# Kernel optimization log

Measured on AMD Instinct MI355X. Metric: run time of the kernel, lower is better.

The kernel has to match this reference:

```python
import jax, jax.numpy as jnp
import numpy as np
import math

N_EMBD = 2048
N_HEAD = 16
HEAD_DIM = N_EMBD // N_HEAD  # 128
K = 8
P = 2
B = 1
T = 2048
EPS = 1e-6


def _rms_norm(x):
    return x * jax.lax.rsqrt(jnp.mean(x * x, axis=-1, keepdims=True) + EPS)


def _rope(x, cos, sin):
    # x: [B, T, H, D]; cos/sin: [T, D//2]
    d = x.shape[-1] // 2
    x1, x2 = x[..., :d], x[..., d:]
    c = cos[None, :, None, :]
    s = sin[None, :, None, :]
    return jnp.concatenate([x1 * c + x2 * s, -x1 * s + x2 * c], axis=-1)


def setup_inputs() -> dict:
    key = jax.random.key(0)
    ks = jax.random.split(key, 8)
    x = jax.random.normal(ks[0], (B, T, N_EMBD), jnp.float32)
    half = HEAD_DIM // 2
    inv_freq = 1.0 / (10000.0 ** (np.arange(half, dtype=np.float32) / half))
    ang = np.arange(T, dtype=np.float32)[:, None] * inv_freq[None, :]
    cos = jnp.asarray(np.cos(ang), jnp.float32)
    sin = jnp.asarray(np.sin(ang), jnp.float32)
    sc = 1.0 / math.sqrt(N_EMBD)
    Wq = jax.random.normal(ks[1], (N_EMBD, N_EMBD), jnp.float32) * sc
    Wk = jax.random.normal(ks[2], (N_EMBD, N_EMBD), jnp.float32) * sc
    Wv = jax.random.normal(ks[3], (N_EMBD, N_EMBD), jnp.float32) * sc
    Wproj = jax.random.normal(ks[4], (N_EMBD, N_EMBD), jnp.float32) * sc
    scd = 1.0 / math.sqrt(HEAD_DIM)
    Wdq = jax.random.normal(ks[5], (K, HEAD_DIM), jnp.float32) * scd
    Wdk = jax.random.normal(ks[6], (K, HEAD_DIM), jnp.float32) * scd
    return {"x": x, "cos": cos, "sin": sin, "Wq": Wq, "Wk": Wk, "Wv": Wv, "Wproj": Wproj, "Wdq": Wdq, "Wdk": Wdk}


def reference(x, cos, sin, Wq, Wk, Wv, Wproj, Wdq, Wdk):
    Bq, Tq, C = x.shape
    q = (x @ Wq.T).reshape(Bq, Tq, N_HEAD, HEAD_DIM)
    k = (x @ Wk.T).reshape(Bq, Tq, N_HEAD, HEAD_DIM)
    v = (x @ Wv.T).reshape(Bq, Tq, N_HEAD, HEAD_DIM)
    q = _rms_norm(_rope(q, cos, sin))
    k = _rms_norm(_rope(k, cos, sin))
    q = jnp.swapaxes(q, 1, 2)  # [B,H,T,D]
    k = jnp.swapaxes(k, 1, 2)
    v = jnp.swapaxes(v, 1, 2)
    # base-p digits in {0..p-1}; p=2 -> bits
    qd = jnp.floor(jax.nn.sigmoid(jnp.einsum('bhtd,kd->bhtk', q, Wdq)) * (P - 0.01)).astype(jnp.int32)
    kd = jnp.floor(jax.nn.sigmoid(jnp.einsum('bhtd,kd->bhtk', k, Wdk)) * (P - 0.01)).astype(jnp.int32)
    # lcp >= K-1  <=>  first K-1 digits all equal; pack them into one code
    pw = (P ** jnp.arange(K - 1)).astype(jnp.int32)  # [K-1]
    qc = jnp.sum(qd[..., : K - 1] * pw, axis=-1)  # [B,H,T]
    kc = jnp.sum(kd[..., : K - 1] * pw, axis=-1)
    lcp_mask = qc[..., :, None] == kc[..., None, :]  # [B,H,Tq,Tk]
    causal = jnp.tril(jnp.ones((Tq, Tq), dtype=bool))
    mask = lcp_mask & causal
    scores = jnp.einsum('bhqd,bhkd->bhqk', q, k) * (1.0 / math.sqrt(HEAD_DIM))
    s = jnp.where(mask, scores, -1e30)
    w = jax.nn.softmax(s, axis=-1)
    w = jnp.where(mask, w, 0.0)
    any_valid = jnp.any(mask, axis=-1, keepdims=True)
    w = jnp.where(any_valid, w, 0.0)  # fully-masked rows -> zero output (torch gives NaN)
    y = jnp.einsum('bhqk,bhkd->bhqd', w, v)
    y = jnp.swapaxes(y, 1, 2).reshape(Bq, Tq, C)
    return y @ Wproj.T
```

## Files before the change

### kernel.cpp

```cpp
#include <hip/hip_runtime.h>
#include <hip/hip_bf16.h>
#include <math.h>

#define T 2048
#define C 2048
#define NH 16
#define HD 128
#define SCALE 0.08838834764831845f
#define WL_CAP 2048
#define MARG 1e-4f

typedef short s16x8 __attribute__((ext_vector_type(8)));
typedef float f32x4 __attribute__((ext_vector_type(4)));
typedef _Float16 f16;
typedef f16 f16x8 __attribute__((ext_vector_type(8)));

__device__ __forceinline__ float wave_sum(float v) {
  #pragma unroll
  for (int o = 32; o > 0; o >>= 1) v += __shfl_xor(v, o, 64);
  return v;
}
__device__ __forceinline__ unsigned short f2bf(float f) {
  unsigned u = __float_as_uint(f);
  u += 0x7FFFu + ((u >> 16) & 1u);
  return (unsigned short)(u >> 16);
}

__global__ __launch_bounds__(256) void to_bf16(const float* __restrict__ in,
                                               unsigned short* __restrict__ outp,
                                               int n4) {
  int i = blockIdx.x * blockDim.x + threadIdx.x;
  const int stride = gridDim.x * blockDim.x;
  for (; i < n4; i += stride) {
    float4 v = ((const float4*)in)[i];
    ushort4 o;
    o.x = f2bf(v.x); o.y = f2bf(v.y); o.z = f2bf(v.z); o.w = f2bf(v.w);
    ((ushort4*)outp)[i] = o;
  }
}

#define SBM 64
#define SBN 128
#define SBK 32
#define PRESC 4096.0f
#define S0F 5.9604644775390625e-8f
#define S1F 2.9103830456733704e-11f
#define S2F 1.4210854715202004e-14f

__device__ __forceinline__ void split8(const float4 v0, const float4 v1,
                                       uint4& hi, uint4& lo) {
  float s[8] = {v0.x * PRESC, v0.y * PRESC, v0.z * PRESC, v0.w * PRESC,
                v1.x * PRESC, v1.y * PRESC, v1.z * PRESC, v1.w * PRESC};
  union { uint4 u; f16 h[8]; } H, L;
  #pragma unroll
  for (int i = 0; i < 8; ++i) {
    f16 h2 = (f16)s[i];
    float d = s[i] - (float)h2;
    H.h[i] = h2;
    L.h[i] = (f16)(d * 2048.0f);
  }
  hi = H.u; lo = L.u;
}

__global__ __launch_bounds__(256, 2) void gemm_qk_split16(const float* __restrict__ A,
                                                          const float* __restrict__ Wq,
                                                          const float* __restrict__ Wk,
                                                          float* __restrict__ Qo,
                                                          float* __restrict__ Ko) {
  const float* __restrict__ Bw = blockIdx.z ? Wk : Wq;
  float* __restrict__ Cc = blockIdx.z ? Ko : Qo;
  __shared__ unsigned short Ah[2][SBM * SBK];
  __shared__ unsigned short Av[2][SBM * SBK];
  __shared__ unsigned short Bh[2][SBN * SBK];
  __shared__ unsigned short Bv[2][SBN * SBK];
  const int tid = threadIdx.x;
  const int bm = blockIdx.x * SBM;
  const int bn = blockIdx.y * SBN;
  const int wv = tid >> 6, lane = tid & 63;
  const int wm = wv & 1, wn = wv >> 1;
  const int lrow = lane & 15, lquad = lane >> 4;

  const int a_row = tid >> 2, qg = tid & 3;
  const int a_qs = qg ^ ((a_row >> 1) & 3);
  const int b_row0 = tid >> 2;
  const int b_qs = qg ^ ((b_row0 >> 1) & 3);

  f32x4 acc[3][2][4];
  #pragma unroll
  for (int g = 0; g < 3; ++g)
    #pragma unroll
    for (int i = 0; i < 2; ++i)
      #pragma unroll
      for (int j = 0; j < 4; ++j) acc[g][i][j] = (f32x4){0.f, 0.f, 0.f, 0.f};

  {
    const float* pA  = A  + (size_t)(bm + a_row) * C + qg * 8;
    const float* pB0 = Bw + (size_t)(bn + b_row0) * C + qg * 8;
    const float* pB1 = Bw + (size_t)(bn + 64 + b_row0) * C + qg * 8;
    uint4 h, l;
    split8(*(const float4*)pA, *(const float4*)(pA + 4), h, l);
    *(uint4*)&Ah[0][a_row * SBK + a_qs * 8] = h;
    *(uint4*)&Av[0][a_row * SBK + a_qs * 8] = l;
    split8(*(const float4*)pB0, *(const float4*)(pB0 + 4), h, l);
    *(uint4*)&Bh[0][b_row0 * SBK + b_qs * 8] = h;
    *(uint4*)&Bv[0][b_row0 * SBK + b_qs * 8] = l;
    split8(*(const float4*)pB1, *(const float4*)(pB1 + 4), h, l);
    *(uint4*)&Bh[0][(64 + b_row0) * SBK + b_qs * 8] = h;
    *(uint4*)&Bv[0][(64 + b_row0) * SBK + b_qs * 8] = l;
  }
  __syncthreads();

  const int niter = C / SBK;
  for (int it = 0; it < niter; ++it) {
    const int cur = it & 1;
    const bool has = (it + 1) < niter;
    float4 a0n, a1n, b00n, b01n, b10n, b11n;
    if (has) {
      const int k0 = (it + 1) * SBK;
      const float* pA  = A  + (size_t)(bm + a_row) * C + k0 + qg * 8;
      const float* pB0 = Bw + (size_t)(bn + b_row0) * C + k0 + qg * 8;
      const float* pB1 = Bw + (size_t)(bn + 64 + b_row0) * C + k0 + qg * 8;
      a0n = *(const float4*)pA;   a1n = *(const float4*)(pA + 4);
      b00n = *(const float4*)pB0; b01n = *(const float4*)(pB0 + 4);
      b10n = *(const float4*)pB1; b11n = *(const float4*)(pB1 + 4);
    }
    f16x8 ah[2], av[2], bh[4], bv[4];
    #pragma unroll
    for (int mi = 0; mi < 2; ++mi) {
      const int r = wm * 32 + mi * 16 + lrow;
      const int q = lquad ^ ((r >> 1) & 3);
      ah[mi] = *(const f16x8*)&Ah[cur][r * SBK + q * 8];
      av[mi] = *(const f16x8*)&Av[cur][r * SBK + q * 8];
    }
    #pragma unroll
    for (int ni = 0; ni < 4; ++ni) {
      const int r = wn * 64 + ni * 16 + lrow;
      const int q = lquad ^ ((r >> 1) & 3);
      bh[ni] = *(const f16x8*)&Bh[cur][r * SBK + q * 8];
      bv[ni] = *(const f16x8*)&Bv[cur][r * SBK + q * 8];
    }
    #pragma unroll
    for (int mi = 0; mi < 2; ++mi)
      #pragma unroll
      for (int ni = 0; ni < 4; ++ni) {
        acc[0][mi][ni] = __builtin_amdgcn_mfma_f32_16x16x32_f16(ah[mi], bh[ni], acc[0][mi][ni], 0, 0, 0);
        acc[1][mi][ni] = __builtin_amdgcn_mfma_f32_16x16x32_f16(ah[mi], bv[ni], acc[1][mi][ni], 0, 0, 0);
        acc[1][mi][ni] = __builtin_amdgcn_mfma_f32_16x16x32_f16(av[mi], bh[ni], acc[1][mi][ni], 0, 0, 0);
        acc[2][mi][ni] = __builtin_amdgcn_mfma_f32_16x16x32_f16(av[mi], bv[ni], acc[2][mi][ni], 0, 0, 0);
      }
    if (has) {
      const int nxt = cur ^ 1;
      uint4 h, l;
      split8(a0n, a1n, h, l);
      *(uint4*)&Ah[nxt][a_row * SBK + a_qs * 8] = h;
      *(uint4*)&Av[nxt][a_row * SBK + a_qs * 8] = l;
      split8(b00n, b01n, h, l);
      *(uint4*)&Bh[nxt][b_row0 * SBK + b_qs * 8] = h;
      *(uint4*)&Bv[nxt][b_row0 * SBK + b_qs * 8] = l;
      split8(b10n, b11n, h, l);
      *(uint4*)&Bh[nxt][(64 + b_row0) * SBK + b_qs * 8] = h;
      *(uint4*)&Bv[nxt][(64 + b_row0) * SBK + b_qs * 8] = l;
    }
    __syncthreads();
  }
  #pragma unroll
  for (int mi = 0; mi < 2; ++mi)
    #pragma unroll
    for (int ni = 0; ni < 4; ++ni)
      #pragma unroll
      for (int r = 0; r < 4; ++r) {
        int row = bm + wm * 32 + mi * 16 + lquad * 4 + r;
        int col = bn + wn * 64 + ni * 16 + lrow;
        float v = acc[0][mi][ni][r] * S0F + (acc[1][mi][ni][r] * S1F + acc[2][mi][ni][r] * S2F);
        Cc[(size_t)row * C + col] = v;
      }
}

#define VBM 64
#define VBN 128
#define VBK 32

__global__ __launch_bounds__(256) void gemm_bf16n(const unsigned short* __restrict__ A,
                                                  const unsigned short* __restrict__ B,
                                                  float* __restrict__ Cc) {
  __shared__ unsigned short Al[2][VBM * VBK];
  __shared__ unsigned short Bl[2][VBN * VBK];
  const int tid = threadIdx.x;
  const int bm = blockIdx.x * VBM;
  const int bn = blockIdx.y * VBN;
  const int wv = tid >> 6, lane = tid & 63;
  const int wm = wv & 1, wn = wv >> 1;
  const int lrow = lane & 15, lquad = lane >> 4;

  const int a_row = tid >> 2, qg = tid & 3;
  const int a_qs = qg ^ ((a_row >> 1) & 3);
  const int b_row0 = tid >> 2;
  const int b_qs = qg ^ ((b_row0 >> 1) & 3);

  f32x4 acc[2][4];
  #pragma unroll
  for (int i = 0; i < 2; ++i)
    #pragma unroll
    for (int j = 0; j < 4; ++j) acc[i][j] = (f32x4){0.f, 0.f, 0.f, 0.f};

  {
    uint4 av = *(const uint4*)(A + (size_t)(bm + a_row) * C + qg * 8);
    uint4 b0 = *(const uint4*)(B + (size_t)(bn + b_row0) * C + qg * 8);
    uint4 b1 = *(const uint4*)(B + (size_t)(bn + 64 + b_row0) * C + qg * 8);
    *(uint4*)&Al[0][a_row * VBK + a_qs * 8] = av;
    *(uint4*)&Bl[0][b_row0 * VBK + b_qs * 8] = b0;
    *(uint4*)&Bl[0][(64 + b_row0) * VBK + b_qs * 8] = b1;
  }
  __syncthreads();

  const int niter = C / VBK;
  for (int it = 0; it < niter; ++it) {
    const int cur = it & 1;
    const bool has = (it + 1) < niter;
    uint4 avn, b0n, b1n;
    if (has) {
      const int k0 = (it + 1) * VBK;
      avn = *(const uint4*)(A + (size_t)(bm + a_row) * C + k0 + qg * 8);
      b0n = *(const uint4*)(B + (size_t)(bn + b_row0) * C + k0 + qg * 8);
      b1n = *(const uint4*)(B + (size_t)(bn + 64 + b_row0) * C + k0 + qg * 8);
    }
    s16x8 af[2], bfr[4];
    #pragma unroll
    for (int mi = 0; mi < 2; ++mi) {
      const int r = wm * 32 + mi * 16 + lrow;
      const int q = lquad ^ ((r >> 1) & 3);
      af[mi] = *(const s16x8*)&Al[cur][r * VBK + q * 8];
    }
    #pragma unroll
    for (int ni = 0; ni < 4; ++ni) {
      const int r = wn * 64 + ni * 16 + lrow;
      const int q = lquad ^ ((r >> 1) & 3);
      bfr[ni] = *(const s16x8*)&Bl[cur][r * VBK + q * 8];
    }
    #pragma unroll
    for (int mi = 0; mi < 2; ++mi)
      #pragma unroll
      for (int ni = 0; ni < 4; ++ni)
        acc[mi][ni] = __builtin_amdgcn_mfma_f32_16x16x32_bf16(af[mi], bfr[ni], acc[mi][ni], 0, 0, 0);
    if (has) {
      const int nxt = cur ^ 1;
      *(uint4*)&Al[nxt][a_row * VBK + a_qs * 8] = avn;
      *(uint4*)&Bl[nxt][b_row0 * VBK + b_qs * 8] = b0n;
      *(uint4*)&Bl[nxt][(64 + b_row0) * VBK + b_qs * 8] = b1n;
    }
    __syncthreads();
  }
  #pragma unroll
  for (int mi = 0; mi < 2; ++mi)
    #pragma unroll
    for (int ni = 0; ni < 4; ++ni)
      #pragma unroll
      for (int r = 0; r < 4; ++r) {
        int row = bm + wm * 32 + mi * 16 + lquad * 4 + r;
        int col = bn + wn * 64 + ni * 16 + lrow;
        Cc[(size_t)row * C + col] = acc[mi][ni][r];
      }
}

__global__ void zero_ctr(int* __restrict__ ctr) {
  if (threadIdx.x == 0) ctr[0] = 0;
}

__global__ __launch_bounds__(256) void rope_fused(float* __restrict__ Qb,
                                                  float* __restrict__ Kb,
                                                  const float* __restrict__ cosb,
                                                  const float* __restrict__ sinb,
                                                  const float* __restrict__ Wdq,
                                                  const float* __restrict__ Wdk,
                                                  int* __restrict__ qcodes,
                                                  int* __restrict__ kcodes,
                                                  int* __restrict__ wl,
                                                  int* __restrict__ ctr) {
  float* __restrict__ buf = blockIdx.y ? Kb : Qb;
  const float* __restrict__ Wd = blockIdx.y ? Wdk : Wdq;
  int* __restrict__ codes = blockIdx.y ? kcodes : qcodes;
  int wave = (blockIdx.x << 2) + (threadIdx.x >> 6);
  int lane = threadIdx.x & 63;
  int t = wave / NH, h = wave % NH;
  size_t base = (size_t)t * C + h * HD;
  float x1 = buf[base + lane];
  float x2 = buf[base + lane + 64];
  float c = cosb[t * 64 + lane];
  float s = sinb[t * 64 + lane];
  float r1 = x1 * c + x2 * s;
  float r2 = x2 * c - x1 * s;
  float ss = wave_sum(r1 * r1 + r2 * r2);
  float inv = 1.0f / sqrtf(ss * (1.0f / 128.0f) + 1e-6f);
  r1 *= inv; r2 *= inv;
  buf[base + lane] = r1;
  buf[base + lane + 64] = r2;
  int code = 0;
  bool marg = false;
  #pragma unroll
  for (int kk = 0; kk < 7; ++kk) {
    float z = r1 * Wd[kk * HD + lane] + r2 * Wd[kk * HD + lane + 64];
    z = wave_sum(z);
    float sig = 1.0f / (1.0f + expf(-z));
    float d = sig * 1.99f - 1.0f;
    if (d >= 0.f) code |= (1 << kk);
    marg |= (fabsf(d) < MARG);
  }
  if (lane == 0) {
    codes[h * T + t] = code;
    if (marg) {
      int i = atomicAdd(ctr, 1);
      if (i < WL_CAP) wl[i] = ((int)blockIdx.y << 15) | (h << 11) | t;
    }
  }
}

__global__ __launch_bounds__(64) void fix_codes(const float* __restrict__ x,
                                                const float* __restrict__ Wq,
                                                const float* __restrict__ Wk,
                                                const float* __restrict__ cosb,
                                                const float* __restrict__ sinb,
                                                const float* __restrict__ Wdq,
                                                const float* __restrict__ Wdk,
                                                int* __restrict__ qc,
                                                int* __restrict__ kc,
                                                const int* __restrict__ wl,
                                                const int* __restrict__ ctr) {
  const int n = min(ctr[0], WL_CAP);
  const int lane = threadIdx.x;
  for (int e = blockIdx.x; e < n; e += gridDim.x) {
    const int ent = wl[e];
    const int isK = ent >> 15;
    const int h = (ent >> 11) & 15;
    const int t = ent & 2047;
    const float* __restrict__ W  = isK ? Wk : Wq;
    const float* __restrict__ Wd = isK ? Wdk : Wdq;
    int* __restrict__ codes = isK ? kc : qc;

    const float* xr = x + (size_t)t * C;
    const float* w0 = W + (size_t)(h * HD + lane) * C;
    const float* w1 = W + (size_t)(h * HD + lane + 64) * C;
    float p0[4] = {0.f, 0.f, 0.f, 0.f};
    float p1[4] = {0.f, 0.f, 0.f, 0.f};
    for (int k = 0; k < C; k += 4) {
      float4 xv = *(const float4*)(xr + k);
      float4 a = *(const float4*)(w0 + k);
      float4 b = *(const float4*)(w1 + k);
      p0[0] += xv.x * a.x; p0[1] += xv.y * a.y;
      p0[2] += xv.z * a.z; p0[3] += xv.w * a.w;
      p1[0] += xv.x * b.x; p1[1] += xv.y * b.y;
      p1[2] += xv.z * b.z; p1[3] += xv.w * b.w;
    }
    float x1 = (p0[0] + p0[1]) + (p0[2] + p0[3]);
    float x2 = (p1[0] + p1[1]) + (p1[2] + p1[3]);
    float c = cosb[t * 64 + lane];
    float s = sinb[t * 64 + lane];
    float r1 = x1 * c + x2 * s;
    float r2 = x2 * c - x1 * s;
    float ss = wave_sum(r1 * r1 + r2 * r2);
    float inv = 1.0f / sqrtf(ss * (1.0f / 128.0f) + 1e-6f);
    r1 *= inv; r2 *= inv;
    int code = 0;
    #pragma unroll
    for (int kk = 0; kk < 7; ++kk) {
      float z = r1 * Wd[kk * HD + lane] + r2 * Wd[kk * HD + lane + 64];
      z = wave_sum(z);
      float sig = 1.0f / (1.0f + expf(-z));
      if (sig * 1.99f >= 1.0f) code |= (1 << kk);
    }
    if (lane == 0) codes[h * T + t] = code;
  }
}

__global__ __launch_bounds__(256) void attn_sparse(const float* __restrict__ Q,
                                                   const float* __restrict__ Kn,
                                                   const float* __restrict__ V,
                                                   const int* __restrict__ qc,
                                                   const int* __restrict__ kc,
                                                   float* __restrict__ Y) {
  const int tid = threadIdx.x;
  const int lane = tid & 63;
  const int wave_id = blockIdx.x * 4 + (tid >> 6);
  const int h = wave_id & (NH - 1);
  const int qrow = wave_id >> 4;
  const size_t hb = (size_t)h * HD;

  const float q0 = Q[(size_t)qrow * C + hb + lane];
  const float q1 = Q[(size_t)qrow * C + hb + lane + 64];
  const int qcode = qc[h * T + qrow];
  const int* kch = kc + h * T;

  float m = -1e30f, l = 0.f, acc0 = 0.f, acc1 = 0.f;

  const int nchunks = (qrow >> 6) + 1;
  int kcj = kch[lane];
  for (int ci = 0; ci < nchunks; ++ci) {
    const int j0 = ci << 6;
    const int cur = kcj;
    if (ci + 1 < nchunks) kcj = kch[j0 + 64 + lane];
    unsigned long long mask = __ballot((cur == qcode) && (j0 + lane <= qrow));
    while (mask) {
      const int j = j0 + (__ffsll((long long)mask) - 1);
      mask &= mask - 1;
      const float* kr = Kn + (size_t)j * C + hb;
      const float* vr = V + (size_t)j * C + hb;
      const float k0v = kr[lane], k1v = kr[lane + 64];
      const float v0 = vr[lane], v1 = vr[lane + 64];
      const float s = wave_sum(q0 * k0v + q1 * k1v) * SCALE;
      const float m_new = fmaxf(m, s);
      const float alpha = __expf(m - m_new);
      const float p = __expf(s - m_new);
      l = l * alpha + p;
      acc0 = acc0 * alpha + p * v0;
      acc1 = acc1 * alpha + p * v1;
      m = m_new;
    }
  }
  const float invl = (l > 0.f) ? 1.0f / l : 0.f;
  Y[(size_t)qrow * C + hb + lane] = acc0 * invl;
  Y[(size_t)qrow * C + hb + lane + 64] = acc1 * invl;
}

extern "C" void kernel_launch(void* const* d_in, const int* in_sizes, int n_in,
                              void* d_out, int out_size, void* d_ws, size_t ws_size,
                              hipStream_t stream) {
  (void)in_sizes; (void)n_in; (void)out_size; (void)ws_size;
  const float* x     = (const float*)d_in[0];
  const float* cosb  = (const float*)d_in[1];
  const float* sinb  = (const float*)d_in[2];
  const float* Wq    = (const float*)d_in[3];
  const float* Wk    = (const float*)d_in[4];
  const float* Wv    = (const float*)d_in[5];
  const float* Wproj = (const float*)d_in[6];
  const float* Wdq   = (const float*)d_in[7];
  const float* Wdk   = (const float*)d_in[8];
  float* out = (float*)d_out;

  float* Kbuf = (float*)d_ws;
  float* V    = Kbuf + (size_t)T * C;
  float* Y    = V    + (size_t)T * C;
  unsigned short* Wbf = (unsigned short*)(Y + (size_t)T * C);
  int*   qc   = (int*)(Wbf + (size_t)T * C);
  int*   kc   = qc + NH * T;
  int*   ctr  = kc + NH * T;
  int*   wl   = ctr + 16;
  unsigned short* xbf = (unsigned short*)Y;
  unsigned short* Ybf = (unsigned short*)Kbuf;
  float* Q    = out;

  const int n4 = T * C / 4;
  to_bf16<<<2048, 256, 0, stream>>>(x, xbf, n4);
  to_bf16<<<2048, 256, 0, stream>>>(Wv, Wbf, n4);
  gemm_bf16n<<<dim3(T / VBM, C / VBN), 256, 0, stream>>>(xbf, Wbf, V);
  gemm_qk_split16<<<dim3(T / SBM, C / SBN, 2), 256, 0, stream>>>(x, Wq, Wk, Q, Kbuf);
  zero_ctr<<<1, 64, 0, stream>>>(ctr);
  rope_fused<<<dim3(T * NH / 4, 2), 256, 0, stream>>>(Q, Kbuf, cosb, sinb, Wdq, Wdk, qc, kc, wl, ctr);
  fix_codes<<<256, 64, 0, stream>>>(x, Wq, Wk, cosb, sinb, Wdq, Wdk, qc, kc, wl, ctr);
  attn_sparse<<<T * NH / 4, 256, 0, stream>>>(Q, Kbuf, V, qc, kc, Y);
  to_bf16<<<2048, 256, 0, stream>>>(Y, Ybf, n4);
  to_bf16<<<2048, 256, 0, stream>>>(Wproj, Wbf, n4);
  gemm_bf16n<<<dim3(T / VBM, C / VBN), 256, 0, stream>>>(Ybf, Wbf, out);
}
```

Measured before the change: 559.4 us.

## Pre-split x, Wq, Wk into f16 hi/lo buffers before Q/K GEMM

```diff
diff --git a/kernel.cpp b/kernel.cpp
--- a/kernel.cpp
+++ b/kernel.cpp
@@ -39,13 +39,139 @@
   }
 }
 
-#define SBM 64
-#define SBN 128
-#define SBK 32
 #define PRESC 4096.0f
 #define S0F 5.9604644775390625e-8f
 #define S1F 2.9103830456733704e-11f
 #define S2F 1.4210854715202004e-14f
+
+__global__ __launch_bounds__(256) void split_f16(const float* __restrict__ in,
+                                                 unsigned short* __restrict__ hip_,
+                                                 unsigned short* __restrict__ lop,
+                                                 int n4) {
+  int i = blockIdx.x * blockDim.x + threadIdx.x;
+  const int stride = gridDim.x * blockDim.x;
+  for (; i < n4; i += stride) {
+    float4 v = ((const float4*)in)[i];
+    float s0 = v.x * PRESC, s1 = v.y * PRESC, s2 = v.z * PRESC, s3 = v.w * PRESC;
+    union { f16 h[4]; ushort4 u; } H, L;
+    H.h[0] = (f16)s0; H.h[1] = (f16)s1; H.h[2] = (f16)s2; H.h[3] = (f16)s3;
+    L.h[0] = (f16)((s0 - (float)H.h[0]) * 2048.0f);
+    L.h[1] = (f16)((s1 - (float)H.h[1]) * 2048.0f);
+    L.h[2] = (f16)((s2 - (float)H.h[2]) * 2048.0f);
+    L.h[3] = (f16)((s3 - (float)H.h[3]) * 2048.0f);
+    ((ushort4*)hip_)[i] = H.u;
+    ((ushort4*)lop)[i] = L.u;
+  }
+}
+
+#define SBM 64
+#define SBN 128
+#define SBK 32
+
+__global__ __launch_bounds__(256, 3) void gemm_qk_pre(const unsigned short* __restrict__ Ahp,
+                                                      const unsigned short* __restrict__ Alp,
+                                                      const unsigned short* __restrict__ Bhp,
+                                                      const unsigned short* __restrict__ Blp,
+                                                      float* __restrict__ Cc) {
+  __shared__ unsigned short Ah[2][SBM * SBK];
+  __shared__ unsigned short Av[2][SBM * SBK];
+  __shared__ unsigned short Bh[2][SBN * SBK];
+  __shared__ unsigned short Bv[2][SBN * SBK];
+  const int tid = threadIdx.x;
+  const int bm = blockIdx.x * SBM;
+  const int bn = blockIdx.y * SBN;
+  const int wv = tid >> 6, lane = tid & 63;
+  const int wm = wv & 1, wn = wv >> 1;
+  const int lrow = lane & 15, lquad = lane >> 4;
+
+  const int a_row = tid >> 2, qg = tid & 3;
+  const int a_qs = qg ^ ((a_row >> 1) & 3);
+  const int b_row0 = tid >> 2;
+  const int b_qs = qg ^ ((b_row0 >> 1) & 3);
+
+  f32x4 acc[2][2][4];
+  #pragma unroll
+  for (int g = 0; g < 2; ++g)
+    #pragma unroll
+    for (int i = 0; i < 2; ++i)
+      #pragma unroll
+      for (int j = 0; j < 4; ++j) acc[g][i][j] = (f32x4){0.f, 0.f, 0.f, 0.f};
+
+  {
+    uint4 aH = *(const uint4*)(Ahp + (size_t)(bm + a_row) * C + qg * 8);
+    uint4 aL = *(const uint4*)(Alp + (size_t)(bm + a_row) * C + qg * 8);
+    uint4 b0H = *(const uint4*)(Bhp + (size_t)(bn + b_row0) * C + qg * 8);
+    uint4 b0L = *(const uint4*)(Blp + (size_t)(bn + b_row0) * C + qg * 8);
+    uint4 b1H = *(const uint4*)(Bhp + (size_t)(bn + 64 + b_row0) * C + qg * 8);
+    uint4 b1L = *(const uint4*)(Blp + (size_t)(bn + 64 + b_row0) * C + qg * 8);
+    *(uint4*)&Ah[0][a_row * SBK + a_qs * 8] = aH;
+    *(uint4*)&Av[0][a_row * SBK + a_qs * 8] = aL;
+    *(uint4*)&Bh[0][b_row0 * SBK + b_qs * 8] = b0H;
+    *(uint4*)&Bv[0][b_row0 * SBK + b_qs * 8] = b0L;
+    *(uint4*)&Bh[0][(64 + b_row0) * SBK + b_qs * 8] = b1H;
+    *(uint4*)&Bv[0][(64 + b_row0) * SBK + b_qs * 8] = b1L;
+  }
+  __syncthreads();
+
+  const int niter = C / SBK;
+  for (int it = 0; it < niter; ++it) {
+    const int cur = it & 1;
+    const bool has = (it + 1) < niter;
+    uint4 aHn, aLn, b0Hn, b0Ln, b1Hn, b1Ln;
+    if (has) {
+      const int k0 = (it + 1) * SBK;
+      aHn = *(const uint4*)(Ahp + (size_t)(bm + a_row) * C + k0 + qg * 8);
+      aLn = *(const uint4*)(Alp + (size_t)(bm + a_row) * C + k0 + qg * 8);
+      b0Hn = *(const uint4*)(Bhp + (size_t)(bn + b_row0) * C + k0 + qg * 8);
+      b0Ln = *(const uint4*)(Blp + (size_t)(bn + b_row0) * C + k0 + qg * 8);
+      b1Hn = *(const uint4*)(Bhp + (size_t)(bn + 64 + b_row0) * C + k0 + qg * 8);
+      b1Ln = *(const uint4*)(Blp + (size_t)(bn + 64 + b_row0) * C + k0 + qg * 8);
+    }
+    f16x8 ah[2], av[2], bh[4], bv[4];
+    #pragma unroll
+    for (int mi = 0; mi < 2; ++mi) {
+      const int r = wm * 32 + mi * 16 + lrow;
+      const int q = lquad ^ ((r >> 1) & 3);
+      ah[mi] = *(const f16x8*)&Ah[cur][r * SBK + q * 8];
+      av[mi] = *(const f16x8*)&Av[cur][r * SBK + q * 8];
+    }
+    #pragma unroll
+    for (int ni = 0; ni < 4; ++ni) {
+      const int r = wn * 64 + ni * 16 + lrow;
+      const int q = lquad ^ ((r >> 1) & 3);
+      bh[ni] = *(const f16x8*)&Bh[cur][r * SBK + q * 8];
+      bv[ni] = *(const f16x8*)&Bv[cur][r * SBK + q * 8];
+    }
+    #pragma unroll
+    for (int mi = 0; mi < 2; ++mi)
+      #pragma unroll
+      for (int ni = 0; ni < 4; ++ni) {
+        acc[0][mi][ni] = __builtin_amdgcn_mfma_f32_16x16x32_f16(ah[mi], bh[ni], acc[0][mi][ni], 0, 0, 0);
+        acc[1][mi][ni] = __builtin_amdgcn_mfma_f32_16x16x32_f16(ah[mi], bv[ni], acc[1][mi][ni], 0, 0, 0);
+        acc[1][mi][ni] = __builtin_amdgcn_mfma_f32_16x16x32_f16(av[mi], bh[ni], acc[1][mi][ni], 0, 0, 0);
+      }
+    if (has) {
+      const int nxt = cur ^ 1;
+      *(uint4*)&Ah[nxt][a_row * SBK + a_qs * 8] = aHn;
+      *(uint4*)&Av[nxt][a_row * SBK + a_qs * 8] = aLn;
+      *(uint4*)&Bh[nxt][b_row0 * SBK + b_qs * 8] = b0Hn;
+      *(uint4*)&Bv[nxt][b_row0 * SBK + b_qs * 8] = b0Ln;
+      *(uint4*)&Bh[nxt][(64 + b_row0) * SBK + b_qs * 8] = b1Hn;
+      *(uint4*)&Bv[nxt][(64 + b_row0) * SBK + b_qs * 8] = b1Ln;
+    }
+    __syncthreads();
+  }
+  #pragma unroll
+  for (int mi = 0; mi < 2; ++mi)
+    #pragma unroll
+    for (int ni = 0; ni < 4; ++ni)
+      #pragma unroll
+      for (int r = 0; r < 4; ++r) {
+        int row = bm + wm * 32 + mi * 16 + lquad * 4 + r;
+        int col = bn + wn * 64 + ni * 16 + lrow;
+        Cc[(size_t)row * C + col] = acc[0][mi][ni][r] * S0F + acc[1][mi][ni][r] * S1F;
+      }
+}
 
 __device__ __forceinline__ void split8(const float4 v0, const float4 v1,
                                        uint4& hi, uint4& lo) {
@@ -423,7 +549,7 @@
 extern "C" void kernel_launch(void* const* d_in, const int* in_sizes, int n_in,
                               void* d_out, int out_size, void* d_ws, size_t ws_size,
                               hipStream_t stream) {
-  (void)in_sizes; (void)n_in; (void)out_size; (void)ws_size;
+  (void)in_sizes; (void)n_in; (void)out_size;
   const float* x     = (const float*)d_in[0];
   const float* cosb  = (const float*)d_in[1];
   const float* sinb  = (const float*)d_in[2];
@@ -435,28 +561,61 @@
   const float* Wdk   = (const float*)d_in[8];
   float* out = (float*)d_out;
 
-  float* Kbuf = (float*)d_ws;
-  float* V    = Kbuf + (size_t)T * C;
-  float* Y    = V    + (size_t)T * C;
-  unsigned short* Wbf = (unsigned short*)(Y + (size_t)T * C);
-  int*   qc   = (int*)(Wbf + (size_t)T * C);
-  int*   kc   = qc + NH * T;
-  int*   ctr  = kc + NH * T;
-  int*   wl   = ctr + 16;
+  const size_t MB = 1024 * 1024;
+  char* ws = (char*)d_ws;
+  float* Kbuf = (float*)ws;
+  float* V    = (float*)(ws + 16 * MB);
+  float* Y    = (float*)(ws + 32 * MB);
+  unsigned short* Wbf = (unsigned short*)(ws + 48 * MB);
   unsigned short* xbf = (unsigned short*)Y;
   unsigned short* Ybf = (unsigned short*)Kbuf;
   float* Q    = out;
 
   const int n4 = T * C / 4;
-  to_bf16<<<2048, 256, 0, stream>>>(x, xbf, n4);
-  to_bf16<<<2048, 256, 0, stream>>>(Wv, Wbf, n4);
-  gemm_bf16n<<<dim3(T / VBM, C / VBN), 256, 0, stream>>>(xbf, Wbf, V);
-  gemm_qk_split16<<<dim3(T / SBM, C / SBN, 2), 256, 0, stream>>>(x, Wq, Wk, Q, Kbuf);
-  zero_ctr<<<1, 64, 0, stream>>>(ctr);
-  rope_fused<<<dim3(T * NH / 4, 2), 256, 0, stream>>>(Q, Kbuf, cosb, sinb, Wdq, Wdk, qc, kc, wl, ctr);
-  fix_codes<<<256, 64, 0, stream>>>(x, Wq, Wk, cosb, sinb, Wdq, Wdk, qc, kc, wl, ctr);
-  attn_sparse<<<T * NH / 4, 256, 0, stream>>>(Q, Kbuf, V, qc, kc, Y);
-  to_bf16<<<2048, 256, 0, stream>>>(Y, Ybf, n4);
-  to_bf16<<<2048, 256, 0, stream>>>(Wproj, Wbf, n4);
-  gemm_bf16n<<<dim3(T / VBM, C / VBN), 256, 0, stream>>>(Ybf, Wbf, out);
-}
+
+  if (ws_size >= (size_t)64 * MB) {
+    unsigned short* xh  = (unsigned short*)Y;
+    unsigned short* xl  = xh + (size_t)T * C;
+    unsigned short* wqh = (unsigned short*)Kbuf;
+    unsigned short* wql = wqh + (size_t)T * C;
+    unsigned short* wkh = Wbf;
+    unsigned short* wkl = (unsigned short*)(ws + 56 * MB);
+    int* qc  = (int*)Wbf;
+    int* kc  = qc + NH * T;
+    int* ctr = kc + NH * T;
+    int* wl  = ctr + 16;
+
+    to_bf16<<<2048, 256, 0, stream>>>(x, xbf, n4);
+    to_bf16<<<2048, 256, 0, stream>>>(Wv, Wbf, n4);
+    gemm_bf16n<<<dim3(T / VBM, C / VBN), 256, 0, stream>>>(xbf, Wbf, V);
+    split_f16<<<2048, 256, 0, stream>>>(x, xh, xl, n4);
+    split_f16<<<2048, 256, 0, stream>>>(Wq, wqh, wql, n4);
+    split_f16<<<2048, 256, 0, stream>>>(Wk, wkh, wkl, n4);
+    gemm_qk_pre<<<dim3(T / SBM, C / SBN), 256, 0, stream>>>(xh, xl, wqh, wql, Q);
+    gemm_qk_pre<<<dim3(T / SBM, C / SBN), 256, 0, stream>>>(xh, xl, wkh, wkl, Kbuf);
+    zero_ctr<<<1, 64, 0, stream>>>(ctr);
+    rope_fused<<<dim3(T * NH / 4, 2), 256, 0, stream>>>(Q, Kbuf, cosb, sinb, Wdq, Wdk, qc, kc, wl, ctr);
+    fix_codes<<<256, 64, 0, stream>>>(x, Wq, Wk, cosb, sinb, Wdq, Wdk, qc, kc, wl, ctr);
+    attn_sparse<<<T * NH / 4, 256, 0, stream>>>(Q, Kbuf, V, qc, kc, Y);
+    to_bf16<<<2048, 256, 0, stream>>>(Y, Ybf, n4);
+    to_bf16<<<2048, 256, 0, stream>>>(Wproj, Wbf, n4);
+    gemm_bf16n<<<dim3(T / VBM, C / VBN), 256, 0, stream>>>(Ybf, Wbf, out);
+  } else {
+    int* qc  = (int*)(Wbf + (size_t)T * C);
+    int* kc  = qc + NH * T;
+    int* ctr = kc + NH * T;
+    int* wl  = ctr + 16;
+
+    to_bf16<<<2048, 256, 0, stream>>>(x, xbf, n4);
+    to_bf16<<<2048, 256, 0, stream>>>(Wv, Wbf, n4);
+    gemm_bf16n<<<dim3(T / VBM, C / VBN), 256, 0, stream>>>(xbf, Wbf, V);
+    gemm_qk_split16<<<dim3(T / SBM, C / SBN, 2), 256, 0, stream>>>(x, Wq, Wk, Q, Kbuf);
+    zero_ctr<<<1, 64, 0, stream>>>(ctr);
+    rope_fused<<<dim3(T * NH / 4, 2), 256, 0, stream>>>(Q, Kbuf, cosb, sinb, Wdq, Wdk, qc, kc, wl, ctr);
+    fix_codes<<<256, 64, 0, stream>>>(x, Wq, Wk, cosb, sinb, Wdq, Wdk, qc, kc, wl, ctr);
+    attn_sparse<<<T * NH / 4, 256, 0, stream>>>(Q, Kbuf, V, qc, kc, Y);
+    to_bf16<<<2048, 256, 0, stream>>>(Y, Ybf, n4);
+    to_bf16<<<2048, 256, 0, stream>>>(Wproj, Wbf, n4);
+    gemm_bf16n<<<dim3(T / VBM, C / VBN), 256, 0, stream>>>(Ybf, Wbf, out);
+  }
+}
```

Result: faster. 504.4 us (-9.8%).
